# Kernel optimization log

Hardware: AMD Instinct MI355X
Metric: run time of the kernel (lower is better)

The kernel has to match this reference:

```python
import jax, jax.numpy as jnp
import numpy as np

B, HG, WG, D, NH, K = 4, 32, 32, 768, 12, 7
HD = D // NH  # 64


def _neigh_idx(H, W, k):
    # NATTEN semantics: 7x7 window centered at the query, shifted (clamped)
    # at borders so every query has exactly k*k neighbors.
    si = np.clip(np.arange(H) - k // 2, 0, H - k)  # [H] window row starts
    sj = np.clip(np.arange(W) - k // 2, 0, W - k)  # [W] window col starts
    ri = si[:, None] + np.arange(k)[None, :]       # [H, k]
    cj = sj[:, None] + np.arange(k)[None, :]       # [W, k]
    idx = ri[:, None, :, None] * W + cj[None, :, None, :]  # [H, W, k, k]
    return jnp.asarray(idx.reshape(H * W, k * k), dtype=jnp.int32)


def setup_inputs() -> dict:
    key = jax.random.key(0)
    ks = jax.random.split(key, 3)
    s = D ** -0.5
    return {
        "x": jax.random.normal(ks[0], (B, HG * WG, D), dtype=jnp.float32),
        "qkv_w": jax.random.normal(ks[1], (3 * D, D), dtype=jnp.float32) * s,
        "qkv_b": jnp.zeros((3 * D,), dtype=jnp.float32),
        "proj_w": jax.random.normal(ks[2], (D, D), dtype=jnp.float32) * s,
        "proj_b": jnp.zeros((D,), dtype=jnp.float32),
    }


def reference(x, qkv_w, qkv_b, proj_w, proj_b):
    b, n, d = x.shape  # n == HG*WG
    idx = _neigh_idx(HG, WG, K)  # [n, K*K] flat neighbor token indices

    qkv = x @ qkv_w.T + qkv_b                      # [b, n, 3d]
    q, k, v = jnp.split(qkv, 3, axis=-1)
    q = q.reshape(b, n, NH, HD) * (HD ** -0.5)     # [b, n, h, hd]
    k = k.reshape(b, n, NH, HD)
    v = v.reshape(b, n, NH, HD)

    kn = jnp.take(k, idx, axis=1)                  # [b, n, 49, h, hd]
    vn = jnp.take(v, idx, axis=1)                  # [b, n, 49, h, hd]

    scores = jnp.einsum('bnhd,bnkhd->bnhk', q, kn)  # [b, n, h, 49]
    attn = jax.nn.softmax(scores, axis=-1)
    out = jnp.einsum('bnhk,bnkhd->bnhd', attn, vn).reshape(b, n, d)
    return out @ proj_w.T + proj_b
```

## Files before the change

### kernel.cpp

```cpp
#include <hip/hip_runtime.h>


typedef __bf16 bf16x8 __attribute__((ext_vector_type(8)));
typedef short s16x4 __attribute__((ext_vector_type(4)));
typedef float f32x4 __attribute__((ext_vector_type(4)));

__device__ __forceinline__ unsigned short f2bf(float f) {
  unsigned u = __float_as_uint(f);
  u += 0x7fffu + ((u >> 16) & 1u);
  return (unsigned short)(u >> 16);
}

template <typename T>
__device__ __forceinline__ void gld_lds16(const T* g, T* l) {
  __builtin_amdgcn_global_load_lds((const __attribute__((address_space(1))) void*)g,
                                   (__attribute__((address_space(3))) void*)l, 16, 0, 0);
}

__global__ void cvt_kernel(const float* __restrict__ x, const float* __restrict__ w1,
                           const float* __restrict__ w2, unsigned short* __restrict__ xo,
                           unsigned short* __restrict__ w1o, unsigned short* __restrict__ w2o) {
  const int n1 = 4096 * 768 / 4;
  const int n2 = 2304 * 768 / 4;
  const int n3 = 768 * 768 / 4;
  int i = blockIdx.x * 256 + threadIdx.x;
  float4 v;
  unsigned short* dst;
  int o;
  if (i < n1) {
    o = i; v = ((const float4*)x)[o]; dst = xo;
  } else if (i < n1 + n2) {
    o = i - n1; v = ((const float4*)w1)[o]; dst = w1o;
  } else if (i < n1 + n2 + n3) {
    o = i - n1 - n2; v = ((const float4*)w2)[o]; dst = w2o;
  } else {
    return;
  }
  ushort4 r;
  r.x = f2bf(v.x); r.y = f2bf(v.y); r.z = f2bf(v.z); r.w = f2bf(v.w);
  ((ushort4*)dst)[o] = r;
}

template <int MODE>
__global__ __launch_bounds__(256) void gemm_bt(const unsigned short* __restrict__ A,
                                               const unsigned short* __restrict__ Bm,
                                               const float* __restrict__ bias,
                                               unsigned short* __restrict__ obf,
                                               unsigned short* __restrict__ vtout,
                                               float* __restrict__ of32,
                                               int M, int N, int Kd) {
  __shared__ __align__(16) unsigned short sA[128 * 32];
  __shared__ __align__(16) unsigned short sB[128 * 32];
  const int tid = threadIdx.x;
  const int lane = tid & 63;
  const int wv = tid >> 6;
  const int m0 = blockIdx.y * 128, n0 = blockIdx.x * 128;
  const int wrow = (wv >> 1) * 64, wcol = (wv & 1) * 64;
  const int lr = lane & 15, lq = lane >> 4;

  f32x4 acc[4][4] = {};

  const unsigned short* gA = A + (size_t)(m0 + (tid >> 2)) * Kd + (tid & 3) * 8;
  const unsigned short* gB = Bm + (size_t)(n0 + (tid >> 2)) * Kd + (tid & 3) * 8;

  for (int k0 = 0; k0 < Kd; k0 += 32) {
    gld_lds16(gA + k0, sA + tid * 8);
    gld_lds16(gA + (size_t)64 * Kd + k0, sA + 2048 + tid * 8);
    gld_lds16(gB + k0, sB + tid * 8);
    gld_lds16(gB + (size_t)64 * Kd + k0, sB + 2048 + tid * 8);
    __syncthreads();

    bf16x8 af[4], bfr[4];
#pragma unroll
    for (int t = 0; t < 4; ++t) {
      af[t] = *(const bf16x8*)(sA + (wrow + t * 16 + lr) * 32 + lq * 8);
      bfr[t] = *(const bf16x8*)(sB + (wcol + t * 16 + lr) * 32 + lq * 8);
    }
#pragma unroll
    for (int im = 0; im < 4; ++im)
#pragma unroll
      for (int in = 0; in < 4; ++in)
        acc[im][in] = __builtin_amdgcn_mfma_f32_16x16x32_bf16(af[im], bfr[in], acc[im][in], 0, 0, 0);
    __syncthreads();
  }

  if (MODE == 0) {
    const int sidx = n0 / 768;
    if (sidx == 2) {
#pragma unroll
      for (int im = 0; im < 4; ++im) {
#pragma unroll
        for (int in = 0; in < 4; ++in) {
          int gn = n0 + wcol + in * 16 + lr;
          int rem = gn - 1536;
          int hh = rem >> 6, dd = gn & 63;
          float bsv = bias[gn];
          int gm0 = m0 + wrow + im * 16 + lq * 4;
          ushort4 pk;
          pk.x = f2bf(acc[im][in][0] + bsv);
          pk.y = f2bf(acc[im][in][1] + bsv);
          pk.z = f2bf(acc[im][in][2] + bsv);
          pk.w = f2bf(acc[im][in][3] + bsv);
          *(ushort4*)(vtout + (size_t)(hh * 64 + dd) * 4096 + gm0) = pk;
        }
      }
    } else {
      const float scale = (sidx == 0) ? 0.18033688f : 1.0f;
#pragma unroll
      for (int im = 0; im < 4; ++im) {
#pragma unroll
        for (int in = 0; in < 4; ++in) {
          int gn = n0 + wcol + in * 16 + lr;
          int rem = gn - sidx * 768;
          int hh = rem >> 6, dd = gn & 63;
          float bsv = bias[gn];
#pragma unroll
          for (int r = 0; r < 4; ++r) {
            int gm = m0 + wrow + im * 16 + lq * 4 + r;
            float val = (acc[im][in][r] + bsv) * scale;
            obf[((size_t)(sidx * 12 + hh) * 4096 + gm) * 64 + dd] = f2bf(val);
          }
        }
      }
    }
  } else {
#pragma unroll
    for (int im = 0; im < 4; ++im) {
#pragma unroll
      for (int in = 0; in < 4; ++in) {
        int gn = n0 + wcol + in * 16 + lr;
        float bsv = bias[gn];
#pragma unroll
        for (int r = 0; r < 4; ++r) {
          int gm = m0 + wrow + im * 16 + lq * 4 + r;
          of32[(size_t)gm * N + gn] = acc[im][in][r] + bsv;
        }
      }
    }
  }
}

__global__ __launch_bounds__(256, 2) void natten_kernel(const unsigned short* __restrict__ qkvt,
                                                        unsigned short* __restrict__ aout) {
  __shared__ __align__(16) unsigned short sQ[64 * 64];
  __shared__ __align__(16) unsigned short sK[256 * 64];
  __shared__ __align__(16) unsigned short sVt[64 * 256];
  const int h = blockIdx.x, ip = blockIdx.y, b = blockIdx.z;
  const int i0 = ip * 2;
  const int tid = threadIdx.x, lane = tid & 63, wv = tid >> 6;
  const int lg = lane >> 4, lm = lane & 15;
  int si0 = i0 - 3; si0 = si0 < 0 ? 0 : si0; if (si0 > 25) si0 = 25;
  const int gb = b * 1024;
  const unsigned short* Qg = qkvt + ((size_t)h * 4096 + gb + i0 * 32) * 64;
  const unsigned short* Kg = qkvt + ((size_t)(12 + h) * 4096 + gb) * 64;
  const unsigned short* Vg = qkvt + (size_t)24 * 4096 * 64 + (size_t)h * 64 * 4096 + gb;

#pragma unroll
  for (int it = 0; it < 2; ++it) {
    int f = it * 256 + tid;
    int q = f >> 3, c16 = f & 7;
    uint4 v = *(const uint4*)(Qg + q * 64 + c16 * 8);
    int s = q & 15;
    *(uint2*)(sQ + q * 64 + ((((c16 << 1)) ^ s) << 2)) = make_uint2(v.x, v.y);
    *(uint2*)(sQ + q * 64 + ((((c16 << 1) | 1) ^ s) << 2)) = make_uint2(v.z, v.w);
  }
#pragma unroll
  for (int it = 0; it < 8; ++it) {
    int f = it * 256 + tid;
    int t = f >> 3, c16 = f & 7;
    int wr = t >> 5, c = t & 31;
    int row = si0 + wr; if (row > 31) row = 31;
    uint4 v = *(const uint4*)(Kg + (row * 32 + c) * 64 + c16 * 8);
    int s = t & 15;
    *(uint2*)(sK + t * 64 + ((((c16 << 1)) ^ s) << 2)) = make_uint2(v.x, v.y);
    *(uint2*)(sK + t * 64 + ((((c16 << 1) | 1) ^ s) << 2)) = make_uint2(v.z, v.w);
  }
#pragma unroll
  for (int it = 0; it < 8; ++it) {
    int f = it * 256 + tid;
    int d = f >> 5, tc16 = f & 31;
    int wr = tc16 >> 2;
    int row = si0 + wr; if (row > 31) row = 31;
    uint4 v = *(const uint4*)(Vg + (size_t)d * 4096 + row * 32 + (tc16 & 3) * 8);
    int s = d & 15;
    *(uint2*)(sVt + d * 256 + ((((tc16 << 1)) ^ s) << 2)) = make_uint2(v.x, v.y);
    *(uint2*)(sVt + d * 256 + ((((tc16 << 1) | 1) ^ s) << 2)) = make_uint2(v.z, v.w);
  }
  __syncthreads();

  const int row_sel = wv >> 1;
  const int jhalf = wv & 1;
  const int i = i0 + row_sel;
  int si_w = i - 3; si_w = si_w < 0 ? 0 : si_w; if (si_w > 25) si_w = 25;
  const int toff = (si_w - si0) * 32;
  const int j = jhalf * 16 + lm;
  int sj = j - 3; sj = sj < 0 ? 0 : sj; if (sj > 25) sj = 25;

  float madd[2][4];
#pragma unroll
  for (int p = 0; p < 2; ++p)
#pragma unroll
    for (int r = 0; r < 4; ++r) {
      int c = p * 16 + lg * 4 + r;
      madd[p][r] = (c >= sj && c <= sj + 6) ? 0.f : -1e30f;
    }

  s16x4 qf[4];
  const int qrow = row_sel * 32 + j;
#pragma unroll
  for (int ks = 0; ks < 4; ++ks)
    qf[ks] = *(const s16x4*)(sQ + qrow * 64 + ((((ks << 2) + lg) ^ (qrow & 15)) << 2));

  f32x4 accS[14];
#pragma unroll
  for (int tt = 0; tt < 14; ++tt) {
    f32x4 a = {0.f, 0.f, 0.f, 0.f};
    const int trow = toff + tt * 16 + lm;
    const unsigned short* kr = sK + trow * 64;
    const int sw = trow & 15;
#pragma unroll
    for (int ks = 0; ks < 4; ++ks) {
      s16x4 kf = *(const s16x4*)(kr + ((((ks << 2) + lg) ^ sw) << 2));
      a = __builtin_amdgcn_mfma_f32_16x16x16bf16_1k(kf, qf[ks], a, 0, 0, 0);
    }
    accS[tt] = a;
  }

  float mx = -3e38f;
#pragma unroll
  for (int tt = 0; tt < 14; ++tt)
#pragma unroll
    for (int r = 0; r < 4; ++r) {
      float v = accS[tt][r] + madd[tt & 1][r];
      accS[tt][r] = v;
      mx = fmaxf(mx, v);
    }
  mx = fmaxf(mx, __shfl_xor(mx, 16, 64));
  mx = fmaxf(mx, __shfl_xor(mx, 32, 64));
  float sum = 0.f;
#pragma unroll
  for (int tt = 0; tt < 14; ++tt)
#pragma unroll
    for (int r = 0; r < 4; ++r) {
      float p = exp2f(accS[tt][r] - mx);
      accS[tt][r] = p;
      sum += p;
    }
  sum += __shfl_xor(sum, 16, 64);
  sum += __shfl_xor(sum, 32, 64);
  const float inv = 1.f / sum;

  s16x4 pf[14];
#pragma unroll
  for (int tt = 0; tt < 14; ++tt) {
    union { unsigned u[2]; s16x4 v; } pk;
    pk.u[0] = ((unsigned)f2bf(accS[tt][1]) << 16) | f2bf(accS[tt][0]);
    pk.u[1] = ((unsigned)f2bf(accS[tt][3]) << 16) | f2bf(accS[tt][2]);
    pf[tt] = pk.v;
  }

  f32x4 accO[4] = {};
  const int choff = toff >> 2;
#pragma unroll
  for (int tt = 0; tt < 14; ++tt) {
    const int c8 = choff + tt * 4 + lg;
#pragma unroll
    for (int nt = 0; nt < 4; ++nt) {
      const int d = nt * 16 + lm;
      s16x4 vf = *(const s16x4*)(sVt + d * 256 + ((c8 ^ (d & 15)) << 2));
      accO[nt] = __builtin_amdgcn_mfma_f32_16x16x16bf16_1k(pf[tt], vf, accO[nt], 0, 0, 0);
    }
  }

  float invr[4];
#pragma unroll
  for (int r = 0; r < 4; ++r) invr[r] = __shfl(inv, lg * 4 + r, 64);

  const int tokbase = gb + i * 32 + jhalf * 16;
#pragma unroll
  for (int nt = 0; nt < 4; ++nt)
#pragma unroll
    for (int r = 0; r < 4; ++r) {
      int tok = tokbase + lg * 4 + r;
      aout[(size_t)tok * 768 + h * 64 + nt * 16 + lm] = f2bf(accO[nt][r] * invr[r]);
    }
}

extern "C" void kernel_launch(void* const* d_in, const int* in_sizes, int n_in,
                              void* d_out, int out_size, void* d_ws, size_t ws_size,
                              hipStream_t stream) {
  const float* x      = (const float*)d_in[0];
  const float* qkv_w  = (const float*)d_in[1];
  const float* qkv_b  = (const float*)d_in[2];
  const float* proj_w = (const float*)d_in[3];
  const float* proj_b = (const float*)d_in[4];
  char* ws = (char*)d_ws;

  unsigned short* xb    = (unsigned short*)(ws);
  unsigned short* wqkv  = (unsigned short*)(ws + 6291456);
  unsigned short* wproj = (unsigned short*)(ws + 9830400);
  unsigned short* qkvt  = (unsigned short*)(ws + 11010048);
  unsigned short* attnb = (unsigned short*)(ws + 29884416);
  unsigned short* vt    = qkvt + (size_t)24 * 4096 * 64;
  float* out = (float*)d_out;

  cvt_kernel<<<5376, 256, 0, stream>>>(x, qkv_w, proj_w, xb, wqkv, wproj);
  gemm_bt<0><<<dim3(18, 32), 256, 0, stream>>>(xb, wqkv, qkv_b, qkvt, vt, nullptr, 4096, 2304, 768);
  natten_kernel<<<dim3(12, 16, 4), 256, 0, stream>>>(qkvt, attnb);
  gemm_bt<1><<<dim3(6, 32), 256, 0, stream>>>(attnb, wproj, proj_b, nullptr, nullptr, out, 4096, 768, 768);
}
```

Measured before the change: 155.5 us.

## Double-buffer GEMM LDS tiles, reorder LDS layout, halve M-tile for projection GEMM

The bf16 GEMM kernel now keeps two LDS buffers and issues the global-to-LDS loads for the next K slice before computing the current one. This is meant to overlap memory latency with MFMA work. Lanes are remapped so each 16-row group is stored contiguously, which is meant to reduce LDS bank conflicts on fragment reads. The kernel is templated on the M tile size, and the output projection GEMM uses 64-row tiles, doubling its grid to 384 blocks to fill more CUs, at the cost of less B-tile reuse and more LDS per block.

```diff
diff --git a/kernel.cpp b/kernel.cpp
--- a/kernel.cpp
+++ b/kernel.cpp
@@ -41,7 +41,7 @@
   ((ushort4*)dst)[o] = r;
 }
 
-template <int MODE>
+template <int MT, int MODE>
 __global__ __launch_bounds__(256) void gemm_bt(const unsigned short* __restrict__ A,
                                                const unsigned short* __restrict__ Bm,
                                                const float* __restrict__ bias,
@@ -49,35 +49,49 @@
                                                unsigned short* __restrict__ vtout,
                                                float* __restrict__ of32,
                                                int M, int N, int Kd) {
-  __shared__ __align__(16) unsigned short sA[128 * 32];
-  __shared__ __align__(16) unsigned short sB[128 * 32];
+  constexpr int BM = MT * 32;
+  __shared__ __align__(16) unsigned short sA[2 * BM * 32];
+  __shared__ __align__(16) unsigned short sB[2 * 128 * 32];
   const int tid = threadIdx.x;
   const int lane = tid & 63;
   const int wv = tid >> 6;
-  const int m0 = blockIdx.y * 128, n0 = blockIdx.x * 128;
-  const int wrow = (wv >> 1) * 64, wcol = (wv & 1) * 64;
+  const int m0 = blockIdx.y * BM, n0 = blockIdx.x * 128;
+  const int wrow = (wv >> 1) * (MT * 16), wcol = (wv & 1) * 64;
   const int lr = lane & 15, lq = lane >> 4;
 
-  f32x4 acc[4][4] = {};
-
-  const unsigned short* gA = A + (size_t)(m0 + (tid >> 2)) * Kd + (tid & 3) * 8;
-  const unsigned short* gB = Bm + (size_t)(n0 + (tid >> 2)) * Kd + (tid & 3) * 8;
-
-  for (int k0 = 0; k0 < Kd; k0 += 32) {
-    gld_lds16(gA + k0, sA + tid * 8);
-    gld_lds16(gA + (size_t)64 * Kd + k0, sA + 2048 + tid * 8);
-    gld_lds16(gB + k0, sB + tid * 8);
-    gld_lds16(gB + (size_t)64 * Kd + k0, sB + 2048 + tid * 8);
-    __syncthreads();
-
-    bf16x8 af[4], bfr[4];
-#pragma unroll
-    for (int t = 0; t < 4; ++t) {
-      af[t] = *(const bf16x8*)(sA + (wrow + t * 16 + lr) * 32 + lq * 8);
-      bfr[t] = *(const bf16x8*)(sB + (wcol + t * 16 + lr) * 32 + lq * 8);
-    }
-#pragma unroll
-    for (int im = 0; im < 4; ++im)
+  f32x4 acc[MT][4] = {};
+
+  const int ls = lane & 15, lc = lane >> 4;
+  const unsigned short* pA  = A  + (size_t)(m0 + wv * 16 + ls) * Kd + lc * 8;
+  const unsigned short* pA2 = A  + (size_t)(m0 + (wv + 4) * 16 + ls) * Kd + lc * 8;
+  const unsigned short* pB  = Bm + (size_t)(n0 + wv * 16 + ls) * Kd + lc * 8;
+  const unsigned short* pB2 = Bm + (size_t)(n0 + (wv + 4) * 16 + ls) * Kd + lc * 8;
+
+  auto stage = [&](int it, int bsel) {
+    const int k0 = it * 32;
+    gld_lds16(pA + k0, sA + bsel * (BM * 32) + tid * 8);
+    if (MT == 4) gld_lds16(pA2 + k0, sA + bsel * (BM * 32) + 2048 + tid * 8);
+    gld_lds16(pB + k0, sB + bsel * 4096 + tid * 8);
+    gld_lds16(pB2 + k0, sB + bsel * 4096 + 2048 + tid * 8);
+  };
+
+  const int nIter = Kd >> 5;
+  stage(0, 0);
+  __syncthreads();
+  for (int it = 0; it < nIter; ++it) {
+    const int cur = it & 1;
+    if (it + 1 < nIter) stage(it + 1, cur ^ 1);
+    const unsigned short* bA = sA + cur * (BM * 32);
+    const unsigned short* bB = sB + cur * 4096;
+    bf16x8 af[MT], bfr[4];
+#pragma unroll
+    for (int t = 0; t < MT; ++t)
+      af[t] = *(const bf16x8*)(bA + ((wrow >> 4) + t) * 512 + lq * 128 + lr * 8);
+#pragma unroll
+    for (int t = 0; t < 4; ++t)
+      bfr[t] = *(const bf16x8*)(bB + ((wcol >> 4) + t) * 512 + lq * 128 + lr * 8);
+#pragma unroll
+    for (int im = 0; im < MT; ++im)
 #pragma unroll
       for (int in = 0; in < 4; ++in)
         acc[im][in] = __builtin_amdgcn_mfma_f32_16x16x32_bf16(af[im], bfr[in], acc[im][in], 0, 0, 0);
@@ -88,7 +102,7 @@
     const int sidx = n0 / 768;
     if (sidx == 2) {
 #pragma unroll
-      for (int im = 0; im < 4; ++im) {
+      for (int im = 0; im < MT; ++im) {
 #pragma unroll
         for (int in = 0; in < 4; ++in) {
           int gn = n0 + wcol + in * 16 + lr;
@@ -107,7 +121,7 @@
     } else {
       const float scale = (sidx == 0) ? 0.18033688f : 1.0f;
 #pragma unroll
-      for (int im = 0; im < 4; ++im) {
+      for (int im = 0; im < MT; ++im) {
 #pragma unroll
         for (int in = 0; in < 4; ++in) {
           int gn = n0 + wcol + in * 16 + lr;
@@ -125,7 +139,7 @@
     }
   } else {
 #pragma unroll
-    for (int im = 0; im < 4; ++im) {
+    for (int im = 0; im < MT; ++im) {
 #pragma unroll
       for (int in = 0; in < 4; ++in) {
         int gn = n0 + wcol + in * 16 + lr;
@@ -305,7 +319,7 @@
   float* out = (float*)d_out;
 
   cvt_kernel<<<5376, 256, 0, stream>>>(x, qkv_w, proj_w, xb, wqkv, wproj);
-  gemm_bt<0><<<dim3(18, 32), 256, 0, stream>>>(xb, wqkv, qkv_b, qkvt, vt, nullptr, 4096, 2304, 768);
+  gemm_bt<4, 0><<<dim3(18, 32), 256, 0, stream>>>(xb, wqkv, qkv_b, qkvt, vt, nullptr, 4096, 2304, 768);
   natten_kernel<<<dim3(12, 16, 4), 256, 0, stream>>>(qkvt, attnb);
-  gemm_bt<1><<<dim3(6, 32), 256, 0, stream>>>(attnb, wproj, proj_b, nullptr, nullptr, out, 4096, 768, 768);
-}
+  gemm_bt<2, 1><<<dim3(6, 64), 256, 0, stream>>>(attnb, wproj, proj_b, nullptr, nullptr, out, 4096, 768, 768);
+}
```

Result: slower. 161.0 us (+3.5%).
